# Kernel tuning notes

Hardware: AMD Instinct MI355X
Metric: run time of the kernel (lower is better)

Reference implementation:

```python
import jax, jax.numpy as jnp
import numpy as np

N, K, D = 32768, 32, 128


def setup_inputs() -> dict:
    key = jax.random.key(0)
    ks = jax.random.split(key, 8)
    return {
        "x1": jax.random.normal(ks[0], (N, D), dtype=jnp.float32),
        "dists_argmax_1": jax.random.randint(ks[1], (N, K), 0, N),
        "dists_max_1": jax.random.uniform(ks[2], (N, K), dtype=jnp.float32),
        "x2": jax.random.normal(ks[3], (N, D), dtype=jnp.float32),
        "dists_argmax_2": jax.random.randint(ks[4], (N, K), 0, N),
        "dists_max_2": jax.random.uniform(ks[5], (N, K), dtype=jnp.float32),
        "w_out": jax.random.normal(ks[6], (1, D), dtype=jnp.float32) * (1.0 / np.sqrt(D)),
        "b_out": jnp.zeros((1,), dtype=jnp.float32),
    }


def _branch(x, idx, dmax, w_out, b_out):
    # anchor gather: [N,K,D]
    anchor = x[idx]
    # mcf 'default': distance-scaled anchor features (self_features unused)
    msgs = dmax[..., None] * anchor  # [N,K,D]
    # linear_out_position then squeeze(-1): [N,K]
    out_pos = jnp.einsum("nkd,d->nk", msgs, w_out[0]) + b_out[0]
    # agg 'mean' over anchor dim: [N,D]
    out_struct = jnp.mean(msgs, axis=1)
    return out_pos, out_struct


def reference(x1, dists_argmax_1, dists_max_1, x2, dists_argmax_2, dists_max_2, w_out, b_out):
    op1, os1 = _branch(x1, dists_argmax_1, dists_max_1, w_out, b_out)
    op2, os2 = _branch(x2, dists_argmax_2, dists_max_2, w_out, b_out)
    return (op1, os1, op2, os2)
```

## Files before the change

### kernel.cpp

```cpp
#include <hip/hip_runtime.h>

#define NN 32768
#define KK 32
#define DD 128

typedef float v2f __attribute__((ext_vector_type(2)));
typedef float v4f __attribute__((ext_vector_type(4)));

__global__ __launch_bounds__(256) void prep_kernel(const float* __restrict__ x1,
                                                   const float* __restrict__ x2,
                                                   const float* __restrict__ w,
                                                   unsigned int* __restrict__ x8,
                                                   float* __restrict__ xw) {
    const int wave = threadIdx.x >> 6;
    const int lane = threadIdx.x & 63;
    const int half = lane >> 5;
    const int c    = lane & 31;
    const int row  = blockIdx.x * 8 + wave * 2 + half;
    const float* x = (row < NN) ? (x1 + (size_t)row * DD)
                                : (x2 + (size_t)(row - NN) * DD);
    const float4 xv = *(const float4*)(x + 4 * c);
    const float4 wv = *(const float4*)(w + 4 * c);

    int packed = __builtin_amdgcn_cvt_pk_fp8_f32(xv.x, xv.y, 0, false);
    packed     = __builtin_amdgcn_cvt_pk_fp8_f32(xv.z, xv.w, packed, true);
    x8[(size_t)row * 32 + c] = (unsigned int)packed;

    float s = xv.x * wv.x + xv.y * wv.y + xv.z * wv.z + xv.w * wv.w;
    #pragma unroll
    for (int m = 16; m >= 1; m >>= 1)
        s += __shfl_xor(s, m, 64);
    if (c == 0) xw[row] = s;
}

__global__ __launch_bounds__(256) void pgnn_main(
    const uint2* __restrict__ x8,
    const float* __restrict__ xw,
    const int* __restrict__ idx1, const float* __restrict__ dm1,
    const int* __restrict__ idx2, const float* __restrict__ dm2,
    const float* __restrict__ b_out,
    float* __restrict__ out)
{
    const int g      = blockIdx.x;
    const int xcd    = g & 7;
    const int branch = xcd >> 2;
    const int nb     = (g >> 3) * 4 + (xcd & 3);

    const uint2* __restrict__ xb  = x8 + (size_t)branch * NN * 16;
    const float* __restrict__ xwb = xw + (size_t)branch * NN;
    const int*   __restrict__ idx = branch ? idx2 : idx1;
    const float* __restrict__ dm  = branch ? dm2  : dm1;
    float* __restrict__ op = out + (size_t)branch * ((size_t)NN * KK + (size_t)NN * DD);
    float* __restrict__ os = op + (size_t)NN * KK;

    __shared__ uint2 s_pair[16][KK + 2];

    const int tid = threadIdx.x;
    const int n0  = nb * 16;

    const float bb = b_out[0];
    #pragma unroll
    for (int j = tid; j < 16 * KK; j += 256) {
        const int rr = j >> 5;
        const int k  = j & 31;
        const size_t off = (size_t)(n0 + rr) * KK + k;
        const int   i  = __builtin_nontemporal_load(idx + off);
        const float dv = __builtin_nontemporal_load(dm + off);
        s_pair[rr][k] = make_uint2((unsigned)i, __float_as_uint(dv));
        __builtin_nontemporal_store(dv * xwb[i] + bb, &op[off]);
    }
    __syncthreads();

    const int sub = tid >> 4;
    const int h   = tid & 15;
    const uint2* __restrict__ prow = s_pair[sub];
    const unsigned hoff = (unsigned)(h << 3);

    float a0=0.f,a1=0.f,a2=0.f,a3=0.f,a4=0.f,a5=0.f,a6=0.f,a7=0.f;
    uint2 ucur[8], unext[8];
    float dcur[8], dnext[8];

    unsigned off0[8];
    #pragma unroll
    for (int j = 0; j < 8; ++j) {
        const uint2 pr = prow[j];
        dcur[j] = __uint_as_float(pr.y);
        off0[j] = (pr.x << 7) | hoff;
    }
    asm volatile(
        "global_load_dwordx2 %0, %8, %16\n\t"
        "global_load_dwordx2 %1, %9, %16\n\t"
        "global_load_dwordx2 %2, %10, %16\n\t"
        "global_load_dwordx2 %3, %11, %16\n\t"
        "global_load_dwordx2 %4, %12, %16\n\t"
        "global_load_dwordx2 %5, %13, %16\n\t"
        "global_load_dwordx2 %6, %14, %16\n\t"
        "global_load_dwordx2 %7, %15, %16"
        : "=&v"(ucur[0]), "=&v"(ucur[1]), "=&v"(ucur[2]), "=&v"(ucur[3]),
          "=&v"(ucur[4]), "=&v"(ucur[5]), "=&v"(ucur[6]), "=&v"(ucur[7])
        : "v"(off0[0]), "v"(off0[1]), "v"(off0[2]), "v"(off0[3]),
          "v"(off0[4]), "v"(off0[5]), "v"(off0[6]), "v"(off0[7]),
          "s"(xb)
        : "memory");

    #pragma unroll
    for (int b = 1; b < KK / 8; ++b) {
        unsigned offn[8];
        #pragma unroll
        for (int j = 0; j < 8; ++j) {
            const uint2 pr = prow[b * 8 + j];
            dnext[j] = __uint_as_float(pr.y);
            offn[j]  = (pr.x << 7) | hoff;
        }
        asm volatile(
            "global_load_dwordx2 %0, %16, %24\n\t"
            "global_load_dwordx2 %1, %17, %24\n\t"
            "global_load_dwordx2 %2, %18, %24\n\t"
            "global_load_dwordx2 %3, %19, %24\n\t"
            "global_load_dwordx2 %4, %20, %24\n\t"
            "global_load_dwordx2 %5, %21, %24\n\t"
            "global_load_dwordx2 %6, %22, %24\n\t"
            "global_load_dwordx2 %7, %23, %24\n\t"
            "s_waitcnt vmcnt(8)"
            : "=&v"(unext[0]), "=&v"(unext[1]), "=&v"(unext[2]), "=&v"(unext[3]),
              "=&v"(unext[4]), "=&v"(unext[5]), "=&v"(unext[6]), "=&v"(unext[7]),
              "+v"(ucur[0]), "+v"(ucur[1]), "+v"(ucur[2]), "+v"(ucur[3]),
              "+v"(ucur[4]), "+v"(ucur[5]), "+v"(ucur[6]), "+v"(ucur[7])
            : "v"(offn[0]), "v"(offn[1]), "v"(offn[2]), "v"(offn[3]),
              "v"(offn[4]), "v"(offn[5]), "v"(offn[6]), "v"(offn[7]),
              "s"(xb)
            : "memory");
        #pragma unroll
        for (int j = 0; j < 8; ++j) {
            const float d = dcur[j];
            const v2f f0 = __builtin_amdgcn_cvt_pk_f32_fp8((int)ucur[j].x, false);
            const v2f f1 = __builtin_amdgcn_cvt_pk_f32_fp8((int)ucur[j].x, true);
            const v2f f2 = __builtin_amdgcn_cvt_pk_f32_fp8((int)ucur[j].y, false);
            const v2f f3 = __builtin_amdgcn_cvt_pk_f32_fp8((int)ucur[j].y, true);
            a0 += d * f0.x; a1 += d * f0.y; a2 += d * f1.x; a3 += d * f1.y;
            a4 += d * f2.x; a5 += d * f2.y; a6 += d * f3.x; a7 += d * f3.y;
        }
        #pragma unroll
        for (int j = 0; j < 8; ++j) { ucur[j] = unext[j]; dcur[j] = dnext[j]; }
    }

    asm volatile("s_waitcnt vmcnt(0)"
                 : "+v"(ucur[0]), "+v"(ucur[1]), "+v"(ucur[2]), "+v"(ucur[3]),
                   "+v"(ucur[4]), "+v"(ucur[5]), "+v"(ucur[6]), "+v"(ucur[7])
                 :
                 : "memory");
    #pragma unroll
    for (int j = 0; j < 8; ++j) {
        const float d = dcur[j];
        const v2f f0 = __builtin_amdgcn_cvt_pk_f32_fp8((int)ucur[j].x, false);
        const v2f f1 = __builtin_amdgcn_cvt_pk_f32_fp8((int)ucur[j].x, true);
        const v2f f2 = __builtin_amdgcn_cvt_pk_f32_fp8((int)ucur[j].y, false);
        const v2f f3 = __builtin_amdgcn_cvt_pk_f32_fp8((int)ucur[j].y, true);
        a0 += d * f0.x; a1 += d * f0.y; a2 += d * f1.x; a3 += d * f1.y;
        a4 += d * f2.x; a5 += d * f2.y; a6 += d * f3.x; a7 += d * f3.y;
    }

    const float inv = 1.0f / KK;
    v4f o0 = { a0 * inv, a1 * inv, a2 * inv, a3 * inv };
    v4f o1 = { a4 * inv, a5 * inv, a6 * inv, a7 * inv };
    float* dst = os + (size_t)(n0 + sub) * DD + h * 8;
    __builtin_nontemporal_store(o0, (v4f*)dst);
    __builtin_nontemporal_store(o1, (v4f*)(dst + 4));
}

__global__ __launch_bounds__(256) void pgnn_fused(
    const float* __restrict__ x1, const int* __restrict__ idx1,
    const float* __restrict__ dm1,
    const float* __restrict__ x2, const int* __restrict__ idx2,
    const float* __restrict__ dm2,
    const float* __restrict__ w, const float* __restrict__ b_out,
    float* __restrict__ out)
{
    const int branch = blockIdx.y;
    const float* __restrict__ x   = branch ? x2   : x1;
    const int*   __restrict__ idx = branch ? idx2 : idx1;
    const float* __restrict__ dm  = branch ? dm2  : dm1;
    float* __restrict__ op = out + (size_t)branch * ((size_t)NN * KK + (size_t)NN * DD);
    float* __restrict__ os = op + (size_t)NN * KK;

    __shared__ int    s_idx[2][KK];
    __shared__ float  s_dm [2][KK];
    __shared__ float  s_dot[2][KK];
    __shared__ float4 s_acc[2][128];

    const int sub = threadIdx.x >> 7;
    const int t   = threadIdx.x & 127;
    const int gg  = t >> 5;
    const int c   = t & 31;
    const int n   = blockIdx.x * 2 + sub;

    if (t < KK) {
        s_idx[sub][t] = idx[(size_t)n * KK + t];
        s_dm [sub][t] = dm [(size_t)n * KK + t];
    }
    const float4 wv = *(const float4*)(w + 4 * c);
    __syncthreads();

    float4 acc = make_float4(0.f, 0.f, 0.f, 0.f);
    #pragma unroll
    for (int k0 = 0; k0 < KK / 4; ++k0) {
        const int   kk  = k0 * 4 + gg;
        const int   r   = s_idx[sub][kk];
        const float dmk = s_dm [sub][kk];
        const float4 v  = *(const float4*)(x + (size_t)r * DD + 4 * c);
        acc.x += dmk * v.x; acc.y += dmk * v.y;
        acc.z += dmk * v.z; acc.w += dmk * v.w;
        float p = v.x * wv.x + v.y * wv.y + v.z * wv.z + v.w * wv.w;
        #pragma unroll
        for (int m = 16; m >= 1; m >>= 1)
            p += __shfl_xor(p, m, 64);
        if (c == 0) s_dot[sub][kk] = p;
    }
    s_acc[sub][t] = acc;
    __syncthreads();

    if (t < KK)
        op[(size_t)n * KK + t] = s_dm[sub][t] * s_dot[sub][t] + b_out[0];
    if (t < 32) {
        const float4 b0 = s_acc[sub][t];
        const float4 b1 = s_acc[sub][32 + t];
        const float4 b2 = s_acc[sub][64 + t];
        const float4 b3 = s_acc[sub][96 + t];
        float4 r;
        r.x = (b0.x + b1.x + b2.x + b3.x) * (1.0f / KK);
        r.y = (b0.y + b1.y + b2.y + b3.y) * (1.0f / KK);
        r.z = (b0.z + b1.z + b2.z + b3.z) * (1.0f / KK);
        r.w = (b0.w + b1.w + b2.w + b3.w) * (1.0f / KK);
        *(float4*)(os + (size_t)n * DD + 4 * t) = r;
    }
}

extern "C" void kernel_launch(void* const* d_in, const int* in_sizes, int n_in,
                              void* d_out, int out_size, void* d_ws, size_t ws_size,
                              hipStream_t stream) {
    const float* x1   = (const float*)d_in[0];
    const int*   idx1 = (const int*)  d_in[1];
    const float* dm1  = (const float*)d_in[2];
    const float* x2   = (const float*)d_in[3];
    const int*   idx2 = (const int*)  d_in[4];
    const float* dm2  = (const float*)d_in[5];
    const float* w    = (const float*)d_in[6];
    const float* b    = (const float*)d_in[7];
    float* out = (float*)d_out;

    const size_t need = (size_t)2 * NN * DD
                      + (size_t)2 * NN * sizeof(float);
    if (ws_size >= need) {
        unsigned int* x8 = (unsigned int*)d_ws;
        float*        xw = (float*)((char*)d_ws + (size_t)2 * NN * DD);
        prep_kernel<<<dim3(2 * NN / 8), dim3(256), 0, stream>>>(x1, x2, w, x8, xw);
        pgnn_main<<<dim3(2 * NN / 16), dim3(256), 0, stream>>>(
            (const uint2*)x8, xw, idx1, dm1, idx2, dm2, b, out);
    } else {
        pgnn_fused<<<dim3(NN / 2, 2), dim3(256), 0, stream>>>(
            x1, idx1, dm1, x2, idx2, dm2, w, b, out);
    }
}
```

Baseline: 137.2 us.

## Cache half-precision xw table in LDS and loop persistent blocks over tiles

The precomputed x·w projection is stored as fp16, and each block copies most of its branch's table (about 62 KB) into LDS, so the out_pos gather reads LDS instead of scattered global memory. The grid shrinks to 512 blocks, each looping over 8 tiles of 16 nodes to amortize that copy. The index and distance are packed into one 32-bit word, with the distance held as fp16. This lowers precision and relies on indices fitting in 16 bits. The large LDS footprint also limits occupancy to about two blocks per CU.

```diff
diff --git a/kernel.cpp b/kernel.cpp
--- a/kernel.cpp
+++ b/kernel.cpp
@@ -1,8 +1,10 @@
 #include <hip/hip_runtime.h>
+#include <hip/hip_fp16.h>
 
 #define NN 32768
 #define KK 32
 #define DD 128
+#define XW_LDS 31712
 
 typedef float v2f __attribute__((ext_vector_type(2)));
 typedef float v4f __attribute__((ext_vector_type(4)));
@@ -11,12 +13,12 @@
                                                    const float* __restrict__ x2,
                                                    const float* __restrict__ w,
                                                    unsigned int* __restrict__ x8,
-                                                   float* __restrict__ xw) {
+                                                   __half* __restrict__ xw16) {
     const int wave = threadIdx.x >> 6;
     const int lane = threadIdx.x & 63;
-    const int half = lane >> 5;
+    const int half_ = lane >> 5;
     const int c    = lane & 31;
-    const int row  = blockIdx.x * 8 + wave * 2 + half;
+    const int row  = blockIdx.x * 8 + wave * 2 + half_;
     const float* x = (row < NN) ? (x1 + (size_t)row * DD)
                                 : (x2 + (size_t)(row - NN) * DD);
     const float4 xv = *(const float4*)(x + 4 * c);
@@ -30,12 +32,12 @@
     #pragma unroll
     for (int m = 16; m >= 1; m >>= 1)
         s += __shfl_xor(s, m, 64);
-    if (c == 0) xw[row] = s;
+    if (c == 0) xw16[row] = __float2half_rn(s);
 }
 
 __global__ __launch_bounds__(256) void pgnn_main(
-    const uint2* __restrict__ x8,
-    const float* __restrict__ xw,
+    const uint2*  __restrict__ x8,
+    const __half* __restrict__ xw16,
     const int* __restrict__ idx1, const float* __restrict__ dm1,
     const int* __restrict__ idx2, const float* __restrict__ dm2,
     const float* __restrict__ b_out,
@@ -44,92 +46,124 @@
     const int g      = blockIdx.x;
     const int xcd    = g & 7;
     const int branch = xcd >> 2;
-    const int nb     = (g >> 3) * 4 + (xcd & 3);
-
-    const uint2* __restrict__ xb  = x8 + (size_t)branch * NN * 16;
-    const float* __restrict__ xwb = xw + (size_t)branch * NN;
-    const int*   __restrict__ idx = branch ? idx2 : idx1;
-    const float* __restrict__ dm  = branch ? dm2  : dm1;
+    const int p      = (g >> 3) * 4 + (xcd & 3);
+
+    const uint2*  __restrict__ xb  = x8   + (size_t)branch * NN * 16;
+    const __half* __restrict__ xwg = xw16 + (size_t)branch * NN;
+    const int*    __restrict__ idx = branch ? idx2 : idx1;
+    const float*  __restrict__ dm  = branch ? dm2  : dm1;
     float* __restrict__ op = out + (size_t)branch * ((size_t)NN * KK + (size_t)NN * DD);
     float* __restrict__ os = op + (size_t)NN * KK;
 
-    __shared__ uint2 s_pair[16][KK + 2];
+    __shared__ __half   s_xw[XW_LDS];
+    __shared__ unsigned s_pairs[16][KK + 1];
 
     const int tid = threadIdx.x;
-    const int n0  = nb * 16;
-
-    const float bb = b_out[0];
-    #pragma unroll
-    for (int j = tid; j < 16 * KK; j += 256) {
-        const int rr = j >> 5;
-        const int k  = j & 31;
-        const size_t off = (size_t)(n0 + rr) * KK + k;
-        const int   i  = __builtin_nontemporal_load(idx + off);
-        const float dv = __builtin_nontemporal_load(dm + off);
-        s_pair[rr][k] = make_uint2((unsigned)i, __float_as_uint(dv));
-        __builtin_nontemporal_store(dv * xwb[i] + bb, &op[off]);
+
+    {
+        const uint4* src = (const uint4*)xwg;
+        uint4* dst = (uint4*)s_xw;
+        for (int j = tid; j < XW_LDS / 8; j += 256) dst[j] = src[j];
     }
     __syncthreads();
 
-    const int sub = tid >> 4;
-    const int h   = tid & 15;
-    const uint2* __restrict__ prow = s_pair[sub];
+    const float bb  = b_out[0];
+    const int  sub  = tid >> 4;
+    const int  h    = tid & 15;
     const unsigned hoff = (unsigned)(h << 3);
 
-    float a0=0.f,a1=0.f,a2=0.f,a3=0.f,a4=0.f,a5=0.f,a6=0.f,a7=0.f;
-    uint2 ucur[8], unext[8];
-    float dcur[8], dnext[8];
-
-    unsigned off0[8];
-    #pragma unroll
-    for (int j = 0; j < 8; ++j) {
-        const uint2 pr = prow[j];
-        dcur[j] = __uint_as_float(pr.y);
-        off0[j] = (pr.x << 7) | hoff;
-    }
-    asm volatile(
-        "global_load_dwordx2 %0, %8, %16\n\t"
-        "global_load_dwordx2 %1, %9, %16\n\t"
-        "global_load_dwordx2 %2, %10, %16\n\t"
-        "global_load_dwordx2 %3, %11, %16\n\t"
-        "global_load_dwordx2 %4, %12, %16\n\t"
-        "global_load_dwordx2 %5, %13, %16\n\t"
-        "global_load_dwordx2 %6, %14, %16\n\t"
-        "global_load_dwordx2 %7, %15, %16"
-        : "=&v"(ucur[0]), "=&v"(ucur[1]), "=&v"(ucur[2]), "=&v"(ucur[3]),
-          "=&v"(ucur[4]), "=&v"(ucur[5]), "=&v"(ucur[6]), "=&v"(ucur[7])
-        : "v"(off0[0]), "v"(off0[1]), "v"(off0[2]), "v"(off0[3]),
-          "v"(off0[4]), "v"(off0[5]), "v"(off0[6]), "v"(off0[7]),
-          "s"(xb)
-        : "memory");
-
-    #pragma unroll
-    for (int b = 1; b < KK / 8; ++b) {
-        unsigned offn[8];
+    for (int t = 0; t < 8; ++t) {
+        const int n0 = p * 128 + t * 16;
+
+        #pragma unroll
+        for (int j = tid; j < 16 * KK; j += 256) {
+            const int rr = j >> 5;
+            const int k  = j & 31;
+            const size_t off = (size_t)(n0 + rr) * KK + k;
+            const int   i  = __builtin_nontemporal_load(idx + off);
+            const float dv = __builtin_nontemporal_load(dm + off);
+            const unsigned short dh = __half_as_ushort(__float2half_rn(dv));
+            s_pairs[rr][k] = (unsigned)i | ((unsigned)dh << 16);
+            const float xwv = (i < XW_LDS) ? __half2float(s_xw[i])
+                                           : __half2float(xwg[i]);
+            __builtin_nontemporal_store(dv * xwv + bb, &op[off]);
+        }
+        __syncthreads();
+
+        const unsigned* __restrict__ prow = s_pairs[sub];
+        float a0=0.f,a1=0.f,a2=0.f,a3=0.f,a4=0.f,a5=0.f,a6=0.f,a7=0.f;
+        uint2 ucur[8], unext[8];
+        float dcur[8], dnext[8];
+
+        unsigned off0[8];
         #pragma unroll
         for (int j = 0; j < 8; ++j) {
-            const uint2 pr = prow[b * 8 + j];
-            dnext[j] = __uint_as_float(pr.y);
-            offn[j]  = (pr.x << 7) | hoff;
+            const unsigned pv = prow[j];
+            dcur[j] = __half2float(__ushort_as_half((unsigned short)(pv >> 16)));
+            off0[j] = ((pv & 0xffffu) << 7) | hoff;
         }
         asm volatile(
-            "global_load_dwordx2 %0, %16, %24\n\t"
-            "global_load_dwordx2 %1, %17, %24\n\t"
-            "global_load_dwordx2 %2, %18, %24\n\t"
-            "global_load_dwordx2 %3, %19, %24\n\t"
-            "global_load_dwordx2 %4, %20, %24\n\t"
-            "global_load_dwordx2 %5, %21, %24\n\t"
-            "global_load_dwordx2 %6, %22, %24\n\t"
-            "global_load_dwordx2 %7, %23, %24\n\t"
-            "s_waitcnt vmcnt(8)"
-            : "=&v"(unext[0]), "=&v"(unext[1]), "=&v"(unext[2]), "=&v"(unext[3]),
-              "=&v"(unext[4]), "=&v"(unext[5]), "=&v"(unext[6]), "=&v"(unext[7]),
-              "+v"(ucur[0]), "+v"(ucur[1]), "+v"(ucur[2]), "+v"(ucur[3]),
-              "+v"(ucur[4]), "+v"(ucur[5]), "+v"(ucur[6]), "+v"(ucur[7])
-            : "v"(offn[0]), "v"(offn[1]), "v"(offn[2]), "v"(offn[3]),
-              "v"(offn[4]), "v"(offn[5]), "v"(offn[6]), "v"(offn[7]),
+            "global_load_dwordx2 %0, %8, %16\n\t"
+            "global_load_dwordx2 %1, %9, %16\n\t"
+            "global_load_dwordx2 %2, %10, %16\n\t"
+            "global_load_dwordx2 %3, %11, %16\n\t"
+            "global_load_dwordx2 %4, %12, %16\n\t"
+            "global_load_dwordx2 %5, %13, %16\n\t"
+            "global_load_dwordx2 %6, %14, %16\n\t"
+            "global_load_dwordx2 %7, %15, %16"
+            : "=&v"(ucur[0]), "=&v"(ucur[1]), "=&v"(ucur[2]), "=&v"(ucur[3]),
+              "=&v"(ucur[4]), "=&v"(ucur[5]), "=&v"(ucur[6]), "=&v"(ucur[7])
+            : "v"(off0[0]), "v"(off0[1]), "v"(off0[2]), "v"(off0[3]),
+              "v"(off0[4]), "v"(off0[5]), "v"(off0[6]), "v"(off0[7]),
               "s"(xb)
             : "memory");
+
+        #pragma unroll
+        for (int b = 1; b < KK / 8; ++b) {
+            unsigned offn[8];
+            #pragma unroll
+            for (int j = 0; j < 8; ++j) {
+                const unsigned pv = prow[b * 8 + j];
+                dnext[j] = __half2float(__ushort_as_half((unsigned short)(pv >> 16)));
+                offn[j]  = ((pv & 0xffffu) << 7) | hoff;
+            }
+            asm volatile(
+                "global_load_dwordx2 %0, %16, %24\n\t"
+                "global_load_dwordx2 %1, %17, %24\n\t"
+                "global_load_dwordx2 %2, %18, %24\n\t"
+                "global_load_dwordx2 %3, %19, %24\n\t"
+                "global_load_dwordx2 %4, %20, %24\n\t"
+                "global_load_dwordx2 %5, %21, %24\n\t"
+                "global_load_dwordx2 %6, %22, %24\n\t"
+                "global_load_dwordx2 %7, %23, %24\n\t"
+                "s_waitcnt vmcnt(8)"
+                : "=&v"(unext[0]), "=&v"(unext[1]), "=&v"(unext[2]), "=&v"(unext[3]),
+                  "=&v"(unext[4]), "=&v"(unext[5]), "=&v"(unext[6]), "=&v"(unext[7]),
+                  "+v"(ucur[0]), "+v"(ucur[1]), "+v"(ucur[2]), "+v"(ucur[3]),
+                  "+v"(ucur[4]), "+v"(ucur[5]), "+v"(ucur[6]), "+v"(ucur[7])
+                : "v"(offn[0]), "v"(offn[1]), "v"(offn[2]), "v"(offn[3]),
+                  "v"(offn[4]), "v"(offn[5]), "v"(offn[6]), "v"(offn[7]),
+                  "s"(xb)
+                : "memory");
+            #pragma unroll
+            for (int j = 0; j < 8; ++j) {
+                const float d = dcur[j];
+                const v2f f0 = __builtin_amdgcn_cvt_pk_f32_fp8((int)ucur[j].x, false);
+                const v2f f1 = __builtin_amdgcn_cvt_pk_f32_fp8((int)ucur[j].x, true);
+                const v2f f2 = __builtin_amdgcn_cvt_pk_f32_fp8((int)ucur[j].y, false);
+                const v2f f3 = __builtin_amdgcn_cvt_pk_f32_fp8((int)ucur[j].y, true);
+                a0 += d * f0.x; a1 += d * f0.y; a2 += d * f1.x; a3 += d * f1.y;
+                a4 += d * f2.x; a5 += d * f2.y; a6 += d * f3.x; a7 += d * f3.y;
+            }
+            #pragma unroll
+            for (int j = 0; j < 8; ++j) { ucur[j] = unext[j]; dcur[j] = dnext[j]; }
+        }
+
+        asm volatile("s_waitcnt vmcnt(0)"
+                     : "+v"(ucur[0]), "+v"(ucur[1]), "+v"(ucur[2]), "+v"(ucur[3]),
+                       "+v"(ucur[4]), "+v"(ucur[5]), "+v"(ucur[6]), "+v"(ucur[7])
+                     :
+                     : "memory");
         #pragma unroll
         for (int j = 0; j < 8; ++j) {
             const float d = dcur[j];
@@ -140,32 +174,15 @@
             a0 += d * f0.x; a1 += d * f0.y; a2 += d * f1.x; a3 += d * f1.y;
             a4 += d * f2.x; a5 += d * f2.y; a6 += d * f3.x; a7 += d * f3.y;
         }
-        #pragma unroll
-        for (int j = 0; j < 8; ++j) { ucur[j] = unext[j]; dcur[j] = dnext[j]; }
-    }
-
-    asm volatile("s_waitcnt vmcnt(0)"
-                 : "+v"(ucur[0]), "+v"(ucur[1]), "+v"(ucur[2]), "+v"(ucur[3]),
-                   "+v"(ucur[4]), "+v"(ucur[5]), "+v"(ucur[6]), "+v"(ucur[7])
-                 :
-                 : "memory");
-    #pragma unroll
-    for (int j = 0; j < 8; ++j) {
-        const float d = dcur[j];
-        const v2f f0 = __builtin_amdgcn_cvt_pk_f32_fp8((int)ucur[j].x, false);
-        const v2f f1 = __builtin_amdgcn_cvt_pk_f32_fp8((int)ucur[j].x, true);
-        const v2f f2 = __builtin_amdgcn_cvt_pk_f32_fp8((int)ucur[j].y, false);
-        const v2f f3 = __builtin_amdgcn_cvt_pk_f32_fp8((int)ucur[j].y, true);
-        a0 += d * f0.x; a1 += d * f0.y; a2 += d * f1.x; a3 += d * f1.y;
-        a4 += d * f2.x; a5 += d * f2.y; a6 += d * f3.x; a7 += d * f3.y;
-    }
-
-    const float inv = 1.0f / KK;
-    v4f o0 = { a0 * inv, a1 * inv, a2 * inv, a3 * inv };
-    v4f o1 = { a4 * inv, a5 * inv, a6 * inv, a7 * inv };
-    float* dst = os + (size_t)(n0 + sub) * DD + h * 8;
-    __builtin_nontemporal_store(o0, (v4f*)dst);
-    __builtin_nontemporal_store(o1, (v4f*)(dst + 4));
+
+        const float inv = 1.0f / KK;
+        v4f o0 = { a0 * inv, a1 * inv, a2 * inv, a3 * inv };
+        v4f o1 = { a4 * inv, a5 * inv, a6 * inv, a7 * inv };
+        float* dst = os + (size_t)(n0 + sub) * DD + h * 8;
+        __builtin_nontemporal_store(o0, (v4f*)dst);
+        __builtin_nontemporal_store(o1, (v4f*)(dst + 4));
+        __syncthreads();
+    }
 }
 
 __global__ __launch_bounds__(256) void pgnn_fused(
@@ -210,11 +227,11 @@
         const float4 v  = *(const float4*)(x + (size_t)r * DD + 4 * c);
         acc.x += dmk * v.x; acc.y += dmk * v.y;
         acc.z += dmk * v.z; acc.w += dmk * v.w;
-        float p = v.x * wv.x + v.y * wv.y + v.z * wv.z + v.w * wv.w;
+        float pp = v.x * wv.x + v.y * wv.y + v.z * wv.z + v.w * wv.w;
         #pragma unroll
         for (int m = 16; m >= 1; m >>= 1)
-            p += __shfl_xor(p, m, 64);
-        if (c == 0) s_dot[sub][kk] = p;
+            pp += __shfl_xor(pp, m, 64);
+        if (c == 0) s_dot[sub][kk] = pp;
     }
     s_acc[sub][t] = acc;
     __syncthreads();
@@ -249,13 +266,13 @@
     float* out = (float*)d_out;
 
     const size_t need = (size_t)2 * NN * DD
-                      + (size_t)2 * NN * sizeof(float);
+                      + (size_t)2 * NN * sizeof(__half);
     if (ws_size >= need) {
-        unsigned int* x8 = (unsigned int*)d_ws;
-        float*        xw = (float*)((char*)d_ws + (size_t)2 * NN * DD);
-        prep_kernel<<<dim3(2 * NN / 8), dim3(256), 0, stream>>>(x1, x2, w, x8, xw);
-        pgnn_main<<<dim3(2 * NN / 16), dim3(256), 0, stream>>>(
-            (const uint2*)x8, xw, idx1, dm1, idx2, dm2, b, out);
+        unsigned int* x8   = (unsigned int*)d_ws;
+        __half*       xw16 = (__half*)((char*)d_ws + (size_t)2 * NN * DD);
+        prep_kernel<<<dim3(2 * NN / 8), dim3(256), 0, stream>>>(x1, x2, w, x8, xw16);
+        pgnn_main<<<dim3(512), dim3(256), 0, stream>>>(
+            (const uint2*)x8, xw16, idx1, dm1, idx2, dm2, b, out);
     } else {
         pgnn_fused<<<dim3(NN / 2, 2), dim3(256), 0, stream>>>(
             x1, idx1, dm1, x2, idx2, dm2, w, b, out);
```

Result: slower. 141.7 us (+3.3%).
